# Optimization experiments

Measured on AMD Instinct MI355X. Metric: run time of the kernel, lower is better.

Reference implementation:

```python
import jax, jax.numpy as jnp
import numpy as np

LN_EPS = 1e-5


def layer_norm(x, gamma, beta):
    mu = jnp.mean(x, axis=-1, keepdims=True)
    var = jnp.var(x, axis=-1, keepdims=True)
    return (x - mu) * jax.lax.rsqrt(var + LN_EPS) * gamma + beta


def setup_inputs() -> dict:
    key = jax.random.key(0)
    ks = jax.random.split(key, 8)
    d = 768
    B, H, W = 8, 32, 32
    s = 1.0 / np.sqrt(d)
    inp = {
        "x": jax.random.normal(ks[0], (B, d, H, W), dtype=jnp.float32),
        "Wq": jax.random.normal(ks[1], (d, d), dtype=jnp.float32) * s,
        "bq": jnp.zeros((d,), jnp.float32),
        "Wk": jax.random.normal(ks[2], (d, d), dtype=jnp.float32) * s,
        "bk": jnp.zeros((d,), jnp.float32),
        "Wv": jax.random.normal(ks[3], (d, d), dtype=jnp.float32) * s,
        "bv": jnp.zeros((d,), jnp.float32),
        "Wo": jax.random.normal(ks[4], (d, d), dtype=jnp.float32) * s,
        "bo": jnp.zeros((d,), jnp.float32),
        "Wg": jax.random.normal(ks[5], (d, d), dtype=jnp.float32) * s,
        "bg": jnp.zeros((d,), jnp.float32),
        "gamma": jnp.ones((d,), jnp.float32),
        "beta": jnp.zeros((d,), jnp.float32),
    }
    return inp


def reference(x, Wq, bq, Wk, bk, Wv, bv, Wo, bo, Wg, bg, gamma, beta):
    n_heads = 12
    B, C, H, W = x.shape
    T = H * W
    d_head = C // n_heads
    # (B, C, H, W) -> (B, T, C)
    xt = x.reshape(B, C, T).transpose(0, 2, 1)
    xn = layer_norm(xt, gamma, beta)
    # torch Linear: x @ W.T + b
    q = xn @ Wq.T + bq
    k = xn @ Wk.T + bk
    v = xn @ Wv.T + bv

    def split_heads(t):
        return t.reshape(B, T, n_heads, d_head).transpose(0, 2, 1, 3)  # (B, nH, T, dh)

    q, k, v = split_heads(q), split_heads(k), split_heads(v)
    scale = 1.0 / np.sqrt(d_head).astype(np.float32)
    scores = jnp.einsum("bhtd,bhsd->bhts", q, k) * scale  # (B, nH, T, T)
    probs = jax.nn.softmax(scores, axis=-1)
    y = jnp.einsum("bhts,bhsd->bhtd", probs, v)  # (B, nH, T, dh)
    # headwise + elementwise gate over full d_model
    gate = jax.nn.sigmoid(xn @ Wg.T + bg)  # (B, T, C)
    gate = gate.reshape(B, T, n_heads, d_head).transpose(0, 2, 1, 3)
    y = y * gate
    y = y.transpose(0, 2, 1, 3).reshape(B, T, C)
    out = y @ Wo.T + bo  # (B, T, C)
    return out.transpose(0, 2, 1).reshape(B, C, H, W)
```

## Files before the change

kernel.cpp:

```cpp
#include <hip/hip_runtime.h>
#include <math.h>

#define B_   8
#define C_   768
#define T_   1024
#define BT_  (B_*T_)
#define WSZ  (C_*C_)

using f16x8 = __attribute__((ext_vector_type(8))) _Float16;
using f32x4 = __attribute__((ext_vector_type(4))) float;
typedef unsigned short u16;

__device__ inline u16 f16b(float x) {
    _Float16 h = (_Float16)x;
    return __builtin_bit_cast(u16, h);
}
__device__ inline float f16f(u16 b) {
    return (float)__builtin_bit_cast(_Float16, b);
}

typedef const __attribute__((address_space(1))) unsigned int gas_uint;
typedef __attribute__((address_space(3))) unsigned int las_uint;
__device__ inline void gld16(const u16* __restrict__ g, u16* l) {
    __builtin_amdgcn_global_load_lds((gas_uint*)g, (las_uint*)l, 16, 0, 0);
}

__global__ __launch_bounds__(256) void wconv_all(
    const float* __restrict__ W0, const float* __restrict__ W1,
    const float* __restrict__ W2, const float* __restrict__ W3,
    const float* __restrict__ W4, u16* __restrict__ wbuf) {
    int mat = blockIdx.y;
    const float* W = (mat == 0) ? W0 : (mat == 1) ? W1 : (mat == 2) ? W2
                   : (mat == 3) ? W3 : W4;
    u16* o = wbuf + (size_t)mat * WSZ;
    int i = (blockIdx.x * 256 + threadIdx.x) * 4;
    float4 w = *(const float4*)(W + i);
    ushort4 h;
    h.x = f16b(w.x);
    h.y = f16b(w.y);
    h.z = f16b(w.z);
    h.w = f16b(w.w);
    *(ushort4*)(o + i) = h;
}

__global__ __launch_bounds__(256) void ln_kernel(const float* __restrict__ x,
                                                 const float* __restrict__ gamma,
                                                 const float* __restrict__ beta,
                                                 u16* __restrict__ xh) {
    int b = blockIdx.y;
    int t0 = blockIdx.x * 16;
    int tid = threadIdx.x;
    int tx = tid & 15;
    int cg = tid >> 4;
    const float* xb = x + (size_t)b * C_ * T_ + t0 + tx;

    float v[48];
    float s = 0.f, sq = 0.f;
    #pragma unroll
    for (int i = 0; i < 48; ++i) {
        float val = xb[(size_t)(i * 16 + cg) * T_];
        v[i] = val; s += val; sq += val * val;
    }
    __shared__ float rs_[16][16], rq_[16][16];
    rs_[cg][tx] = s;
    rq_[cg][tx] = sq;
    __syncthreads();
    __shared__ float mu_[16], rstd_[16];
    if (tid < 16) {
        float S = 0.f, Q = 0.f;
        #pragma unroll
        for (int k = 0; k < 16; ++k) { S += rs_[k][tid]; Q += rq_[k][tid]; }
        float mu = S * (1.0f / 768.0f);
        float var = Q * (1.0f / 768.0f) - mu * mu;
        mu_[tid] = mu;
        rstd_[tid] = 1.0f / sqrtf(var + 1e-5f);
    }
    __syncthreads();
    float mu = mu_[tx], rstd = rstd_[tx];
    __shared__ u16 Lt[16][776];
    #pragma unroll
    for (int i = 0; i < 48; ++i) {
        int c = i * 16 + cg;
        Lt[tx][c] = f16b((v[i] - mu) * rstd * gamma[c] + beta[c]);
    }
    __syncthreads();
    size_t obase = ((size_t)b * 1024 + t0) * C_;
    #pragma unroll
    for (int st = 0; st < 12; ++st) {
        int idx = st * 256 + tid;
        int t = idx / 192, c4 = idx % 192;
        *(ushort4*)(xh + obase + (size_t)t * C_ + c4 * 4) = *(ushort4*)&Lt[t][c4 * 4];
    }
}

__global__ __launch_bounds__(256, 3) void qkvg_mfma(
    const u16* __restrict__ xh, const u16* __restrict__ wmats,
    const float* __restrict__ bq, const float* __restrict__ bk,
    const float* __restrict__ bv, const float* __restrict__ bg,
    u16* __restrict__ qh, u16* __restrict__ kh,
    u16* __restrict__ vth, u16* __restrict__ g) {
    int bx = blockIdx.x;
    int by = blockIdx.y;
    int mat = by / 6;
    int n0  = (by % 6) * 128;
    int m0  = bx * 128;
    const u16* Wh = wmats + (size_t)mat * WSZ;
    const float* bias = (mat == 0) ? bq : (mat == 1) ? bk : (mat == 2) ? bv : bg;

    __shared__ __attribute__((aligned(16))) u16 Ah[2 * 4096], Bh[2 * 4096];

    int tid  = threadIdx.x;
    int lane = tid & 63, wid = tid >> 6;
    int wm = (wid & 1) * 64, wn = (wid >> 1) * 64;
    int fr = lane & 15, rq = (lane >> 4) * 4;

    f32x4 acc[4][4];
    #pragma unroll
    for (int i = 0; i < 4; ++i)
        #pragma unroll
        for (int j = 0; j < 4; ++j)
            acc[i][j] = (f32x4){0.f, 0.f, 0.f, 0.f};

    int ba = (wm >> 4), bb2 = (wn >> 4);

    int f0 = 2 * wid;
    const u16* gA0 = xh + (size_t)(m0 + f0 * 16 + fr) * 768 + (lane >> 4) * 8;
    const u16* gA1 = gA0 + (size_t)16 * 768;
    const u16* gB0 = Wh + (size_t)(n0 + f0 * 16 + fr) * 768 + (lane >> 4) * 8;
    const u16* gB1 = gB0 + (size_t)16 * 768;
    int la0 = f0 * 512 + lane * 8;
    int la1 = la0 + 512;

    #define STAGE(T, BUF) do { int kk0 = (T) * 32; int bo_ = (BUF) * 4096; \
        gld16(gA0 + kk0, Ah + bo_ + la0); \
        gld16(gA1 + kk0, Ah + bo_ + la1); \
        gld16(gB0 + kk0, Bh + bo_ + la0); \
        gld16(gB1 + kk0, Bh + bo_ + la1); \
    } while (0)

    STAGE(0, 0);
    __syncthreads();
    int cur = 0;
    for (int t = 0; t < 24; ++t) {
        int nxt = cur ^ 1;
        if (t + 1 < 24) STAGE(t + 1, nxt);
        int cb = cur * 4096;
        f16x8 fah[4], fbh[4];
        #pragma unroll
        for (int i = 0; i < 4; ++i) {
            fah[i] = *(const f16x8*)(Ah + cb + (ba + i) * 512 + lane * 8);
            fbh[i] = *(const f16x8*)(Bh + cb + (bb2 + i) * 512 + lane * 8);
        }
        if (mat == 2) {
            #pragma unroll
            for (int mi = 0; mi < 4; ++mi)
                #pragma unroll
                for (int ni = 0; ni < 4; ++ni)
                    acc[mi][ni] = __builtin_amdgcn_mfma_f32_16x16x32_f16(fbh[ni], fah[mi], acc[mi][ni], 0, 0, 0);
        } else {
            #pragma unroll
            for (int mi = 0; mi < 4; ++mi)
                #pragma unroll
                for (int ni = 0; ni < 4; ++ni)
                    acc[mi][ni] = __builtin_amdgcn_mfma_f32_16x16x32_f16(fah[mi], fbh[ni], acc[mi][ni], 0, 0, 0);
        }
        __syncthreads();
        cur = nxt;
    }
    #undef STAGE
    if (mat == 2) {
        int bb = m0 >> 10;
        #pragma unroll
        for (int mi = 0; mi < 4; ++mi) {
            int tok = m0 + wm + mi * 16 + fr;
            int tl  = tok & 1023;
            #pragma unroll
            for (int ni = 0; ni < 4; ++ni) {
                #pragma unroll
                for (int rg = 0; rg < 4; ++rg) {
                    int ch = n0 + wn + ni * 16 + rq + rg;
                    float val = acc[mi][ni][rg] + bias[ch];
                    size_t addr = ((size_t)((bb * 12 + (ch >> 6)) * 64 + (ch & 63))) * 1024 + tl;
                    vth[addr] = f16b(val);
                }
            }
        }
    } else {
        u16* oh = (mat == 0) ? qh : (mat == 1) ? kh : g;
        float scale = (mat == 0) ? 0.125f : 1.0f;
        #pragma unroll
        for (int ni = 0; ni < 4; ++ni) {
            int col = n0 + wn + ni * 16 + fr;
            float bb = bias[col];
            #pragma unroll
            for (int mi = 0; mi < 4; ++mi) {
                int row = m0 + wm + mi * 16 + rq;
                #pragma unroll
                for (int rg = 0; rg < 4; ++rg) {
                    float val = (acc[mi][ni][rg] + bb) * scale;
                    oh[(size_t)(row + rg) * 768 + col] = f16b(val);
                }
            }
        }
    }
}

__global__ __launch_bounds__(256, 3) void attn_mfma(
    const u16* __restrict__ qhg, const u16* __restrict__ khg,
    const u16* __restrict__ vthg, const u16* __restrict__ gbf,
    u16* __restrict__ yh) {
    int qt = blockIdx.x;
    int h  = blockIdx.y;
    int b  = blockIdx.z;
    __shared__ __attribute__((aligned(16))) u16 Kh[2 * 4096], Vh[2 * 4096];
    __shared__ u16 Ps[64 * 72];
    int tid = threadIdx.x;
    int lane = tid & 63, w = tid >> 6;
    int fr = lane & 15, quad = lane >> 4, fq = quad * 8;

    size_t qbaseA = ((size_t)(b * 1024 + qt * 128)) * 768 + h * 64;
    size_t qbaseB = qbaseA + (size_t)64 * 768;
    size_t kbase = ((size_t)(b * 1024)) * 768 + h * 64;
    size_t vbase = ((size_t)((b * 12 + h) * 64)) * 1024;

    f16x8 aqA[2], aqB[2];
    #pragma unroll
    for (int kk = 0; kk < 2; ++kk) {
        size_t ro = (size_t)(w * 16 + fr) * 768 + kk * 32 + fq;
        aqA[kk] = *(const f16x8*)(qhg + qbaseA + ro);
        aqB[kk] = *(const f16x8*)(qhg + qbaseB + ro);
    }

    float m_A = -1e30f, l_A = 0.0f, m_B = -1e30f, l_B = 0.0f;
    f32x4 OA[4], OB[4];
    #pragma unroll
    for (int i = 0; i < 4; ++i) {
        OA[i] = (f32x4){0.f, 0.f, 0.f, 0.f};
        OB[i] = (f32x4){0.f, 0.f, 0.f, 0.f};
    }

    int f0 = 2 * w;
    int f1 = f0 + 1;
    const u16* kgA = khg + kbase + (size_t)((f0 & 3) * 16 + fr) * 768 + (f0 >> 2) * 32 + (lane >> 4) * 8;
    const u16* kgB = khg + kbase + (size_t)((f1 & 3) * 16 + fr) * 768 + (f1 >> 2) * 32 + (lane >> 4) * 8;
    const u16* vgA = vthg + vbase + (size_t)((f0 & 3) * 16 + fr) * 1024 + (f0 >> 2) * 32 + (lane >> 4) * 8;
    const u16* vgB = vthg + vbase + (size_t)((f1 & 3) * 16 + fr) * 1024 + (f1 >> 2) * 32 + (lane >> 4) * 8;
    int ldA = f0 * 512 + lane * 8;
    int ldB = ldA + 512;

    #define STAGE(ST, BUF) do { \
        size_t ko = (size_t)(ST) * 49152; \
        size_t vo = (size_t)(ST) * 64; \
        int bo_ = (BUF) * 4096; \
        gld16(kgA + ko, Kh + bo_ + ldA); \
        gld16(kgB + ko, Kh + bo_ + ldB); \
        gld16(vgA + vo, Vh + bo_ + ldA); \
        gld16(vgB + vo, Vh + bo_ + ldB); \
    } while (0)

    #define STRIP(AQ, MS, LS, OACC) do { \
        f32x4 sacc[4]; \
        _Pragma("unroll") \
        for (int nt = 0; nt < 4; ++nt) sacc[nt] = (f32x4){0.f, 0.f, 0.f, 0.f}; \
        _Pragma("unroll") \
        for (int nt = 0; nt < 4; ++nt) \
            _Pragma("unroll") \
            for (int kk = 0; kk < 2; ++kk) { \
                f16x8 kb = *(const f16x8*)(Kh + cur * 4096 + (kk * 4 + nt) * 512 + lane * 8); \
                sacc[nt] = __builtin_amdgcn_mfma_f32_16x16x32_f16(kb, AQ[kk], sacc[nt], 0, 0, 0); \
            } \
        float mx = -1e30f; \
        _Pragma("unroll") \
        for (int nt = 0; nt < 4; ++nt) \
            _Pragma("unroll") \
            for (int rg = 0; rg < 4; ++rg) mx = fmaxf(mx, sacc[nt][rg]); \
        mx = fmaxf(mx, __shfl_xor(mx, 16)); \
        mx = fmaxf(mx, __shfl_xor(mx, 32)); \
        float mn = fmaxf(MS, mx); \
        float al = __expf(MS - mn); \
        MS = mn; \
        float rs = 0.0f; \
        _Pragma("unroll") \
        for (int nt = 0; nt < 4; ++nt) \
            _Pragma("unroll") \
            for (int rg = 0; rg < 4; ++rg) { \
                float p = __expf(sacc[nt][rg] - mn); \
                sacc[nt][rg] = p; \
                rs += p; \
            } \
        rs += __shfl_xor(rs, 16); \
        rs += __shfl_xor(rs, 32); \
        LS = LS * al + rs; \
        int prow = (w * 16 + fr) * 72; \
        _Pragma("unroll") \
        for (int nt = 0; nt < 4; ++nt) { \
            ushort4 hp; \
            hp.x = f16b(sacc[nt][0]); \
            hp.y = f16b(sacc[nt][1]); \
            hp.z = f16b(sacc[nt][2]); \
            hp.w = f16b(sacc[nt][3]); \
            *(ushort4*)&Ps[prow + nt * 16 + quad * 4] = hp; \
        } \
        float alr[4]; \
        _Pragma("unroll") \
        for (int rg = 0; rg < 4; ++rg) alr[rg] = __shfl(al, quad * 4 + rg, 16); \
        _Pragma("unroll") \
        for (int dn = 0; dn < 4; ++dn) \
            _Pragma("unroll") \
            for (int rg = 0; rg < 4; ++rg) OACC[dn][rg] *= alr[rg]; \
        _Pragma("unroll") \
        for (int kk = 0; kk < 2; ++kk) { \
            f16x8 pa = *(const f16x8*)&Ps[(w * 16 + fr) * 72 + fq + kk * 32]; \
            _Pragma("unroll") \
            for (int dn = 0; dn < 4; ++dn) { \
                f16x8 vb = *(const f16x8*)(Vh + cur * 4096 + (kk * 4 + dn) * 512 + lane * 8); \
                OACC[dn] = __builtin_amdgcn_mfma_f32_16x16x32_f16(pa, vb, OACC[dn], 0, 0, 0); \
            } \
        } \
    } while (0)

    STAGE(0, 0);
    __syncthreads();
    int cur = 0;
    for (int st = 0; st < 16; ++st) {
        int nxt = cur ^ 1;
        if (st + 1 < 16) STAGE(st + 1, nxt);
        STRIP(aqA, m_A, l_A, OA);
        STRIP(aqB, m_B, l_B, OB);
        __syncthreads();
        cur = nxt;
    }
    #undef STAGE
    #undef STRIP
    float invA[4], invB[4];
    #pragma unroll
    for (int rg = 0; rg < 4; ++rg) {
        invA[rg] = 1.0f / __shfl(l_A, quad * 4 + rg, 16);
        invB[rg] = 1.0f / __shfl(l_B, quad * 4 + rg, 16);
    }
    int tokA0 = b * 1024 + qt * 128 + w * 16;
    #pragma unroll
    for (int dn = 0; dn < 4; ++dn) {
        int ch = h * 64 + dn * 16 + fr;
        #pragma unroll
        for (int rg = 0; rg < 4; ++rg) {
            int tok = tokA0 + quad * 4 + rg;
            float gv = f16f(gbf[(size_t)tok * 768 + ch]);
            float sg = 1.0f / (1.0f + __expf(-gv));
            yh[(size_t)tok * 768 + ch] = f16b(OA[dn][rg] * invA[rg] * sg);
            int tok2 = tok + 64;
            float gv2 = f16f(gbf[(size_t)tok2 * 768 + ch]);
            float sg2 = 1.0f / (1.0f + __expf(-gv2));
            yh[(size_t)tok2 * 768 + ch] = f16b(OB[dn][rg] * invB[rg] * sg2);
        }
    }
}

__global__ __launch_bounds__(256, 3) void out_mfma(
    const u16* __restrict__ yh, const u16* __restrict__ woh,
    const float* __restrict__ bo, float* __restrict__ out) {
    int bx = blockIdx.x;
    int by = blockIdx.y;
    int m0 = bx * 128;
    int n0 = by * 128;

    __shared__ __attribute__((aligned(16))) u16 Ah[2 * 4096], Bh[2 * 4096];

    int tid  = threadIdx.x;
    int lane = tid & 63, wid = tid >> 6;
    int wm = (wid & 1) * 64, wn = (wid >> 1) * 64;
    int fr = lane & 15, rq = (lane >> 4) * 4;

    f32x4 acc[4][4];
    #pragma unroll
    for (int i = 0; i < 4; ++i)
        #pragma unroll
        for (int j = 0; j < 4; ++j)
            acc[i][j] = (f32x4){0.f, 0.f, 0.f, 0.f};

    int ba = (wm >> 4), bb2 = (wn >> 4);

    int f0 = 2 * wid;
    const u16* gA0 = woh + (size_t)(m0 + f0 * 16 + fr) * 768 + (lane >> 4) * 8;
    const u16* gA1 = gA0 + (size_t)16 * 768;
    const u16* gB0 = yh + (size_t)(n0 + f0 * 16 + fr) * 768 + (lane >> 4) * 8;
    const u16* gB1 = gB0 + (size_t)16 * 768;
    int la0 = f0 * 512 + lane * 8;
    int la1 = la0 + 512;

    #define STAGE(T, BUF) do { int kk0 = (T) * 32; int bo_ = (BUF) * 4096; \
        gld16(gA0 + kk0, Ah + bo_ + la0); \
        gld16(gA1 + kk0, Ah + bo_ + la1); \
        gld16(gB0 + kk0, Bh + bo_ + la0); \
        gld16(gB1 + kk0, Bh + bo_ + la1); \
    } while (0)

    STAGE(0, 0);
    __syncthreads();
    int cur = 0;
    for (int t = 0; t < 24; ++t) {
        int nxt = cur ^ 1;
        if (t + 1 < 24) STAGE(t + 1, nxt);
        int cb = cur * 4096;
        f16x8 fah[4], fbh[4];
        #pragma unroll
        for (int i = 0; i < 4; ++i) {
            fah[i] = *(const f16x8*)(Ah + cb + (ba + i) * 512 + lane * 8);
            fbh[i] = *(const f16x8*)(Bh + cb + (bb2 + i) * 512 + lane * 8);
        }
        #pragma unroll
        for (int mi = 0; mi < 4; ++mi)
            #pragma unroll
            for (int ni = 0; ni < 4; ++ni)
                acc[mi][ni] = __builtin_amdgcn_mfma_f32_16x16x32_f16(fah[mi], fbh[ni], acc[mi][ni], 0, 0, 0);
        __syncthreads();
        cur = nxt;
    }
    #undef STAGE
    int bb = n0 >> 10;
    #pragma unroll
    for (int ni = 0; ni < 4; ++ni) {
        int colg = n0 + wn + ni * 16 + fr;
        int tl = colg & 1023;
        #pragma unroll
        for (int mi = 0; mi < 4; ++mi) {
            int row = m0 + wm + mi * 16 + rq;
            #pragma unroll
            for (int rg = 0; rg < 4; ++rg) {
                float val = acc[mi][ni][rg] + bo[row + rg];
                out[((size_t)bb * 768 + row + rg) * 1024 + tl] = val;
            }
        }
    }
}

extern "C" void kernel_launch(void* const* d_in, const int* in_sizes, int n_in,
                              void* d_out, int out_size, void* d_ws, size_t ws_size,
                              hipStream_t stream) {
    const float* x     = (const float*)d_in[0];
    const float* Wq    = (const float*)d_in[1];
    const float* bq    = (const float*)d_in[2];
    const float* Wk    = (const float*)d_in[3];
    const float* bk    = (const float*)d_in[4];
    const float* Wv    = (const float*)d_in[5];
    const float* bv    = (const float*)d_in[6];
    const float* Wo    = (const float*)d_in[7];
    const float* bo    = (const float*)d_in[8];
    const float* Wg    = (const float*)d_in[9];
    const float* bg    = (const float*)d_in[10];
    const float* gamma = (const float*)d_in[11];
    const float* beta  = (const float*)d_in[12];
    float* out = (float*)d_out;

    const size_t S = (size_t)BT_ * C_;
    u16* xn   = (u16*)d_ws;
    u16* qh   = xn + S;
    u16* kh   = qh + S;
    u16* vth  = kh + S;
    u16* g_bf = vth + S;
    u16* wbuf = g_bf + S;
    u16* y_h  = xn;

    wconv_all<<<dim3(WSZ / 1024, 5), 256, 0, stream>>>(Wq, Wk, Wv, Wg, Wo, wbuf);
    ln_kernel<<<dim3(64, 8), 256, 0, stream>>>(x, gamma, beta, xn);
    qkvg_mfma<<<dim3(64, 24), 256, 0, stream>>>(xn, wbuf, bq, bk, bv, bg,
                                                qh, kh, vth, g_bf);
    attn_mfma<<<dim3(8, 12, 8), 256, 0, stream>>>(qh, kh, vth, g_bf, y_h);
    out_mfma<<<dim3(6, 64), 256, 0, stream>>>(y_h, wbuf + (size_t)4 * WSZ, bo, out);
}
```

Measured before the change: 276.5 us.

## Load GEMM operands directly from global into registers, dropping LDS staging

Both projection GEMM kernels (QKVG and output) stop staging A/B tiles through double-buffered LDS with global_load_lds and barriers. Each wave now reads its MFMA fragments straight from global memory, prefetching B one k-step ahead in registers, and launch bounds drop from 3 to 2 blocks per CU to make room for the extra registers. This removes the LDS round trip and the block barriers, but each wave reloads data that other waves share, which raises global and L2 traffic, and occupancy falls.

```diff
diff --git a/kernel.cpp b/kernel.cpp
--- a/kernel.cpp
+++ b/kernel.cpp
@@ -93,7 +93,7 @@
     }
 }
 
-__global__ __launch_bounds__(256, 3) void qkvg_mfma(
+__global__ __launch_bounds__(256, 2) void qkvg_mfma(
     const u16* __restrict__ xh, const u16* __restrict__ wmats,
     const float* __restrict__ bq, const float* __restrict__ bk,
     const float* __restrict__ bv, const float* __restrict__ bg,
@@ -107,8 +107,6 @@
     const u16* Wh = wmats + (size_t)mat * WSZ;
     const float* bias = (mat == 0) ? bq : (mat == 1) ? bk : (mat == 2) ? bv : bg;
 
-    __shared__ __attribute__((aligned(16))) u16 Ah[2 * 4096], Bh[2 * 4096];
-
     int tid  = threadIdx.x;
     int lane = tid & 63, wid = tid >> 6;
     int wm = (wid & 1) * 64, wn = (wid >> 1) * 64;
@@ -121,53 +119,46 @@
         for (int j = 0; j < 4; ++j)
             acc[i][j] = (f32x4){0.f, 0.f, 0.f, 0.f};
 
-    int ba = (wm >> 4), bb2 = (wn >> 4);
-
-    int f0 = 2 * wid;
-    const u16* gA0 = xh + (size_t)(m0 + f0 * 16 + fr) * 768 + (lane >> 4) * 8;
-    const u16* gA1 = gA0 + (size_t)16 * 768;
-    const u16* gB0 = Wh + (size_t)(n0 + f0 * 16 + fr) * 768 + (lane >> 4) * 8;
-    const u16* gB1 = gB0 + (size_t)16 * 768;
-    int la0 = f0 * 512 + lane * 8;
-    int la1 = la0 + 512;
-
-    #define STAGE(T, BUF) do { int kk0 = (T) * 32; int bo_ = (BUF) * 4096; \
-        gld16(gA0 + kk0, Ah + bo_ + la0); \
-        gld16(gA1 + kk0, Ah + bo_ + la1); \
-        gld16(gB0 + kk0, Bh + bo_ + la0); \
-        gld16(gB1 + kk0, Bh + bo_ + la1); \
-    } while (0)
-
-    STAGE(0, 0);
-    __syncthreads();
-    int cur = 0;
-    for (int t = 0; t < 24; ++t) {
-        int nxt = cur ^ 1;
-        if (t + 1 < 24) STAGE(t + 1, nxt);
-        int cb = cur * 4096;
-        f16x8 fah[4], fbh[4];
-        #pragma unroll
-        for (int i = 0; i < 4; ++i) {
-            fah[i] = *(const f16x8*)(Ah + cb + (ba + i) * 512 + lane * 8);
-            fbh[i] = *(const f16x8*)(Bh + cb + (bb2 + i) * 512 + lane * 8);
-        }
-        if (mat == 2) {
-            #pragma unroll
-            for (int mi = 0; mi < 4; ++mi)
-                #pragma unroll
-                for (int ni = 0; ni < 4; ++ni)
-                    acc[mi][ni] = __builtin_amdgcn_mfma_f32_16x16x32_f16(fbh[ni], fah[mi], acc[mi][ni], 0, 0, 0);
-        } else {
-            #pragma unroll
-            for (int mi = 0; mi < 4; ++mi)
-                #pragma unroll
-                for (int ni = 0; ni < 4; ++ni)
-                    acc[mi][ni] = __builtin_amdgcn_mfma_f32_16x16x32_f16(fah[mi], fbh[ni], acc[mi][ni], 0, 0, 0);
-        }
-        __syncthreads();
-        cur = nxt;
-    }
-    #undef STAGE
+    const u16* Ar = xh + (size_t)(m0 + wm + fr) * 768 + (lane >> 4) * 8;
+    const u16* Br = Wh + (size_t)(n0 + wn + fr) * 768 + (lane >> 4) * 8;
+
+    f16x8 pB0[4], pB1[4];
+    #define LOADB(dst, T) do { int kk0 = (T) * 32; \
+        dst[0] = *(const f16x8*)(Br + kk0); \
+        dst[1] = *(const f16x8*)(Br + 12288 + kk0); \
+        dst[2] = *(const f16x8*)(Br + 24576 + kk0); \
+        dst[3] = *(const f16x8*)(Br + 36864 + kk0); \
+    } while (0)
+    #define STEP(BREG, T) do { int kk0 = (T) * 32; \
+        f16x8 fa[4]; \
+        fa[0] = *(const f16x8*)(Ar + kk0); \
+        fa[1] = *(const f16x8*)(Ar + 12288 + kk0); \
+        fa[2] = *(const f16x8*)(Ar + 24576 + kk0); \
+        fa[3] = *(const f16x8*)(Ar + 36864 + kk0); \
+        if (mat == 2) { \
+            _Pragma("unroll") \
+            for (int mi = 0; mi < 4; ++mi) \
+                _Pragma("unroll") \
+                for (int ni = 0; ni < 4; ++ni) \
+                    acc[mi][ni] = __builtin_amdgcn_mfma_f32_16x16x32_f16(BREG[ni], fa[mi], acc[mi][ni], 0, 0, 0); \
+        } else { \
+            _Pragma("unroll") \
+            for (int mi = 0; mi < 4; ++mi) \
+                _Pragma("unroll") \
+                for (int ni = 0; ni < 4; ++ni) \
+                    acc[mi][ni] = __builtin_amdgcn_mfma_f32_16x16x32_f16(fa[mi], BREG[ni], acc[mi][ni], 0, 0, 0); \
+        } \
+    } while (0)
+
+    LOADB(pB0, 0);
+    for (int t = 0; t < 24; t += 2) {
+        LOADB(pB1, t + 1);
+        STEP(pB0, t);
+        if (t + 2 < 24) LOADB(pB0, t + 2);
+        STEP(pB1, t + 1);
+    }
+    #undef LOADB
+    #undef STEP
     if (mat == 2) {
         int bb = m0 >> 10;
         #pragma unroll
@@ -356,7 +347,7 @@
     }
 }
 
-__global__ __launch_bounds__(256, 3) void out_mfma(
+__global__ __launch_bounds__(256, 2) void out_mfma(
     const u16* __restrict__ yh, const u16* __restrict__ woh,
     const float* __restrict__ bo, float* __restrict__ out) {
     int bx = blockIdx.x;
@@ -364,8 +355,6 @@
     int m0 = bx * 128;
     int n0 = by * 128;
 
-    __shared__ __attribute__((aligned(16))) u16 Ah[2 * 4096], Bh[2 * 4096];
-
     int tid  = threadIdx.x;
     int lane = tid & 63, wid = tid >> 6;
     int wm = (wid & 1) * 64, wn = (wid >> 1) * 64;
@@ -378,45 +367,38 @@
         for (int j = 0; j < 4; ++j)
             acc[i][j] = (f32x4){0.f, 0.f, 0.f, 0.f};
 
-    int ba = (wm >> 4), bb2 = (wn >> 4);
-
-    int f0 = 2 * wid;
-    const u16* gA0 = woh + (size_t)(m0 + f0 * 16 + fr) * 768 + (lane >> 4) * 8;
-    const u16* gA1 = gA0 + (size_t)16 * 768;
-    const u16* gB0 = yh + (size_t)(n0 + f0 * 16 + fr) * 768 + (lane >> 4) * 8;
-    const u16* gB1 = gB0 + (size_t)16 * 768;
-    int la0 = f0 * 512 + lane * 8;
-    int la1 = la0 + 512;
-
-    #define STAGE(T, BUF) do { int kk0 = (T) * 32; int bo_ = (BUF) * 4096; \
-        gld16(gA0 + kk0, Ah + bo_ + la0); \
-        gld16(gA1 + kk0, Ah + bo_ + la1); \
-        gld16(gB0 + kk0, Bh + bo_ + la0); \
-        gld16(gB1 + kk0, Bh + bo_ + la1); \
-    } while (0)
-
-    STAGE(0, 0);
-    __syncthreads();
-    int cur = 0;
-    for (int t = 0; t < 24; ++t) {
-        int nxt = cur ^ 1;
-        if (t + 1 < 24) STAGE(t + 1, nxt);
-        int cb = cur * 4096;
-        f16x8 fah[4], fbh[4];
-        #pragma unroll
-        for (int i = 0; i < 4; ++i) {
-            fah[i] = *(const f16x8*)(Ah + cb + (ba + i) * 512 + lane * 8);
-            fbh[i] = *(const f16x8*)(Bh + cb + (bb2 + i) * 512 + lane * 8);
-        }
-        #pragma unroll
-        for (int mi = 0; mi < 4; ++mi)
-            #pragma unroll
-            for (int ni = 0; ni < 4; ++ni)
-                acc[mi][ni] = __builtin_amdgcn_mfma_f32_16x16x32_f16(fah[mi], fbh[ni], acc[mi][ni], 0, 0, 0);
-        __syncthreads();
-        cur = nxt;
-    }
-    #undef STAGE
+    const u16* Ar = woh + (size_t)(m0 + wm + fr) * 768 + (lane >> 4) * 8;
+    const u16* Br = yh + (size_t)(n0 + wn + fr) * 768 + (lane >> 4) * 8;
+
+    f16x8 pB0[4], pB1[4];
+    #define LOADB(dst, T) do { int kk0 = (T) * 32; \
+        dst[0] = *(const f16x8*)(Br + kk0); \
+        dst[1] = *(const f16x8*)(Br + 12288 + kk0); \
+        dst[2] = *(const f16x8*)(Br + 24576 + kk0); \
+        dst[3] = *(const f16x8*)(Br + 36864 + kk0); \
+    } while (0)
+    #define STEP(BREG, T) do { int kk0 = (T) * 32; \
+        f16x8 fa[4]; \
+        fa[0] = *(const f16x8*)(Ar + kk0); \
+        fa[1] = *(const f16x8*)(Ar + 12288 + kk0); \
+        fa[2] = *(const f16x8*)(Ar + 24576 + kk0); \
+        fa[3] = *(const f16x8*)(Ar + 36864 + kk0); \
+        _Pragma("unroll") \
+        for (int mi = 0; mi < 4; ++mi) \
+            _Pragma("unroll") \
+            for (int ni = 0; ni < 4; ++ni) \
+                acc[mi][ni] = __builtin_amdgcn_mfma_f32_16x16x32_f16(fa[mi], BREG[ni], acc[mi][ni], 0, 0, 0); \
+    } while (0)
+
+    LOADB(pB0, 0);
+    for (int t = 0; t < 24; t += 2) {
+        LOADB(pB1, t + 1);
+        STEP(pB0, t);
+        if (t + 2 < 24) LOADB(pB0, t + 2);
+        STEP(pB1, t + 1);
+    }
+    #undef LOADB
+    #undef STEP
     int bb = n0 >> 10;
     #pragma unroll
     for (int ni = 0; ni < 4; ++ni) {
```

Measured after the change: 349.6 us. +26.4%, slower.
